# Kernel optimization log

Hardware: AMD Instinct MI355X
Metric: run time of the kernel (lower is better)

The kernel has to match this reference:

```python
import jax, jax.numpy as jnp
import numpy as np

V = 50257   # vocab / ouput_size
H = 1024    # hidden_size
L = 4096    # encoder length
NL = 2      # num_layers


def setup_inputs() -> dict:
    key = jax.random.key(0)
    ks = jax.random.split(key, 20)
    s = 0.02
    f32 = jnp.float32
    return {
        "input": jax.random.randint(ks[0], (1, 1), 0, V),
        "hidden_state": jax.random.normal(ks[1], (NL, 1, H), f32),
        "enc_outputs": jax.random.normal(ks[2], (L, H), f32),
        # parameters
        "emb": jax.random.normal(ks[3], (V, H), f32) * s,
        "Wq": jax.random.normal(ks[4], (H, H), f32) * s,
        "Wk": jax.random.normal(ks[5], (H, H), f32) * s,
        "wv": jax.random.normal(ks[6], (H, 1), f32) * s,
        "W_ih0": jax.random.normal(ks[7], (3 * H, 2 * H), f32) * s,
        "W_hh0": jax.random.normal(ks[8], (3 * H, H), f32) * s,
        "b_ih0": jnp.zeros((3 * H,), f32),
        "b_hh0": jnp.zeros((3 * H,), f32),
        "W_ih1": jax.random.normal(ks[9], (3 * H, H), f32) * s,
        "W_hh1": jax.random.normal(ks[10], (3 * H, H), f32) * s,
        "b_ih1": jnp.zeros((3 * H,), f32),
        "b_hh1": jnp.zeros((3 * H,), f32),
        "Wd": jax.random.normal(ks[11], (H, V), f32) * s,
        "bd": jnp.zeros((V,), f32),
    }


def _gru_step(x, h, W_ih, W_hh, b_ih, b_hh):
    # PyTorch GRU cell: gates ordered (reset, update, new)
    gi = W_ih @ x + b_ih          # [3H]
    gh = W_hh @ h + b_hh          # [3H]
    i_r, i_z, i_n = jnp.split(gi, 3)
    h_r, h_z, h_n = jnp.split(gh, 3)
    r = jax.nn.sigmoid(i_r + h_r)
    z = jax.nn.sigmoid(i_z + h_z)
    n = jnp.tanh(i_n + r * h_n)
    return (1.0 - z) * n + z * h


def reference(input, hidden_state, enc_outputs, emb, Wq, Wk, wv,
              W_ih0, W_hh0, b_ih0, b_hh0, W_ih1, W_hh1, b_ih1, b_hh1,
              Wd, bd):
    # embedding + (dropout p=0 is identity) + relu  -> [H]
    emb_vec = jax.nn.relu(emb[input[0, 0]])
    # additive attention: query = last-layer hidden [H], keys/values = enc [L,H]
    query = hidden_state[-1, 0]
    feat = jnp.tanh(query @ Wq + enc_outputs @ Wk)   # [L,H] (broadcast add)
    scores = feat @ wv                               # [L,1]
    attn = jax.nn.softmax(scores, axis=0)            # softmax over L
    context = jnp.sum(attn * enc_outputs, axis=0)    # [H]
    # single-step 2-layer GRU on concat(context, embedded) -> [2H]
    x = jnp.concatenate([context, emb_vec])
    h0n = _gru_step(x, hidden_state[0, 0], W_ih0, W_hh0, b_ih0, b_hh0)
    h1n = _gru_step(h0n, hidden_state[1, 0], W_ih1, W_hh1, b_ih1, b_hh1)
    # dense + log_softmax over vocab
    logits = h1n @ Wd + bd                           # [V]
    logp = jax.nn.log_softmax(logits)[None, :]       # [1,V]
    new_hidden = jnp.stack([h0n, h1n])[:, None, :]   # [NL,1,H]
    return logp, new_hidden
```

## Files before the change

### kernel.cpp

```cpp
#include <hip/hip_runtime.h>
#include <hip/hip_bf16.h>

#define H  1024
#define L  4096
#define V  50257

#define OFF_QW     0
#define OFF_SCORES 1024
#define OFF_X      5120
#define OFF_GI0    7168
#define OFF_GH0    10240
#define OFF_GI1    13312
#define OFF_GH1    16384
#define OFF_LOGITS 19456
#define OFF_PMAX   (OFF_LOGITS + V)
#define OFF_PSUM   (OFF_PMAX + 256)
#define ZERO_FLOATS (OFF_LOGITS + V)
#define OFF_WKT_BYTES 283008

typedef __bf16 bf8   __attribute__((ext_vector_type(8)));
typedef float  f32x16 __attribute__((ext_vector_type(16)));

__device__ inline unsigned int pack_bf16x2(float lo, float hi) {
    unsigned int ulo = __builtin_bit_cast(unsigned int, lo);
    unsigned int uhi = __builtin_bit_cast(unsigned int, hi);
    return ((uhi + 0x8000u) & 0xFFFF0000u) | ((ulo + 0x8000u) >> 16);
}
__device__ inline unsigned short cvt_bf16(float f) {
    unsigned int u = __builtin_bit_cast(unsigned int, f);
    return (unsigned short)((u + 0x8000u) >> 16);
}

__global__ __launch_bounds__(256) void k_prep(const int* __restrict__ tok,
                                              const float* __restrict__ emb,
                                              const float* __restrict__ hid,
                                              const float* __restrict__ Wq,
                                              const float* __restrict__ Wk,
                                              const float* __restrict__ Whh0,
                                              const float* __restrict__ bhh0,
                                              const float* __restrict__ Whh1,
                                              const float* __restrict__ bhh1,
                                              float* __restrict__ ws,
                                              unsigned short* __restrict__ wkT) {
    __shared__ float tile[32][33];
    const int b = blockIdx.x, t = threadIdx.x;
    if (b < 4) {
        int j = b * 256 + t;
        float v = emb[(size_t)tok[0] * H + j];
        ws[OFF_X + H + j] = fmaxf(v, 0.f);
    } else if (b < 68) {
        int bb = b - 4;
        int j = (bb & 3) * 256 + t;
        int i0 = (bb >> 2) * 64;
        const float* q = hid + H;
        float acc = 0.f;
#pragma unroll 8
        for (int i = i0; i < i0 + 64; ++i) acc += q[i] * Wq[i * H + j];
        atomicAdd(&ws[OFF_QW + j], acc);
    } else if (b < 1092) {
        int tt = b - 68;
        int tk = tt & 31, tn = tt >> 5;
        int c = t & 31, r0 = t >> 5;
#pragma unroll
        for (int rr = 0; rr < 4; ++rr) {
            int r = r0 + rr * 8;
            tile[r][c] = Wk[(size_t)(tk * 32 + r) * H + tn * 32 + c];
        }
        __syncthreads();
#pragma unroll
        for (int rr = 0; rr < 4; ++rr) {
            int rn = r0 + rr * 8;
            wkT[(size_t)(tn * 32 + rn) * H + tk * 32 + c] = cvt_bf16(tile[c][rn]);
        }
    } else {
        bool l1 = (b >= 1860);
        int row  = (b - (l1 ? 1860 : 1092)) * 4 + (t >> 6);
        int lane = t & 63;
        const float*  W  = l1 ? Whh1 : Whh0;
        const float*  bi = l1 ? bhh1 : bhh0;
        const float4* hv = (const float4*)(l1 ? hid + H : hid);
        const float4* Wr = (const float4*)(W + (size_t)row * H);
        float acc = 0.f;
#pragma unroll
        for (int c = lane; c < H / 4; c += 64) {
            float4 w = Wr[c], x = hv[c];
            acc += w.x * x.x + w.y * x.y + w.z * x.z + w.w * x.w;
        }
#pragma unroll
        for (int off = 32; off; off >>= 1) acc += __shfl_down(acc, off);
        if (lane == 0) ws[(l1 ? OFF_GH1 : OFF_GH0) + row] = acc + bi[row];
    }
}

__global__ __launch_bounds__(256) void k_gemm_scores(const float* __restrict__ enc,
                                                     const unsigned short* __restrict__ wkT,
                                                     const float* __restrict__ wv,
                                                     float* __restrict__ ws) {
    __shared__ unsigned short As[64][40];
    __shared__ unsigned short Bs[128][40];
    const int t = threadIdx.x, lane = t & 63, w = t >> 6;
    const int m0 = blockIdx.x * 64, n0 = blockIdx.y * 128;

    f32x16 acc0 = {}, acc1 = {};

    const int ar = t >> 2, akq = (t & 3) * 8;
    const int bn = t >> 1, bkh = (t & 1) * 16;

    const int r0 = (w & 1) * 32, c0 = (w >> 1) * 64;
    const int mrow = r0 + (lane & 31);
    const int nrow0 = c0 + (lane & 31), nrow1 = nrow0 + 32;

    for (int k0 = 0; k0 < H; k0 += 32) {
        float4 fa = *(const float4*)(enc + (size_t)(m0 + ar) * H + k0 + akq);
        float4 fb = *(const float4*)(enc + (size_t)(m0 + ar) * H + k0 + akq + 4);
        uint4 wb0 = *(const uint4*)(wkT + (size_t)(n0 + bn) * H + k0 + bkh);
        uint4 wb1 = *(const uint4*)(wkT + (size_t)(n0 + bn) * H + k0 + bkh + 8);
        __syncthreads();
        uint4 pa;
        pa.x = pack_bf16x2(fa.x, fa.y); pa.y = pack_bf16x2(fa.z, fa.w);
        pa.z = pack_bf16x2(fb.x, fb.y); pa.w = pack_bf16x2(fb.z, fb.w);
        *(uint4*)&As[ar][akq] = pa;
        *(uint4*)&Bs[bn][bkh] = wb0;
        *(uint4*)&Bs[bn][bkh + 8] = wb1;
        __syncthreads();
#pragma unroll
        for (int kk = 0; kk < 2; ++kk) {
            int kb = kk * 16 + (lane >> 5) * 8;
            bf8 a  = *(const bf8*)&As[mrow][kb];
            bf8 b0 = *(const bf8*)&Bs[nrow0][kb];
            bf8 b1 = *(const bf8*)&Bs[nrow1][kb];
            acc0 = __builtin_amdgcn_mfma_f32_32x32x16_bf16(a, b0, acc0, 0, 0, 0);
            acc1 = __builtin_amdgcn_mfma_f32_32x32x16_bf16(a, b1, acc1, 0, 0, 0);
        }
    }

    const int n_a = n0 + nrow0, n_b = n0 + nrow1;
    float qwa = ws[OFF_QW + n_a], qwb = ws[OFF_QW + n_b];
    float wva = wv[n_a], wvb = wv[n_b];
    const int rbase = m0 + r0 + 4 * (lane >> 5);
#pragma unroll
    for (int reg = 0; reg < 16; ++reg) {
        float s = tanhf(acc0[reg] + qwa) * wva + tanhf(acc1[reg] + qwb) * wvb;
#pragma unroll
        for (int msk = 1; msk < 32; msk <<= 1) s += __shfl_xor(s, msk);
        if ((lane & 31) == 0) {
            int l = rbase + (reg & 3) + 8 * (reg >> 2);
            atomicAdd(&ws[OFF_SCORES + l], s);
        }
    }
}

__global__ __launch_bounds__(256) void k_context(const float* __restrict__ enc,
                                                 float* __restrict__ ws) {
    __shared__ float red[4];
    __shared__ float ps[128];
    const int t = threadIdx.x;
    const float* sc = ws + OFF_SCORES;

    float m = -1e30f;
#pragma unroll
    for (int i = 0; i < 16; ++i) m = fmaxf(m, sc[t + i * 256]);
#pragma unroll
    for (int msk = 1; msk < 64; msk <<= 1) m = fmaxf(m, __shfl_xor(m, msk));
    if ((t & 63) == 0) red[t >> 6] = m;
    __syncthreads();
    m = fmaxf(fmaxf(red[0], red[1]), fmaxf(red[2], red[3]));
    __syncthreads();

    float s = 0.f;
#pragma unroll
    for (int i = 0; i < 16; ++i) s += expf(sc[t + i * 256] - m);
#pragma unroll
    for (int msk = 1; msk < 64; msk <<= 1) s += __shfl_xor(s, msk);
    if ((t & 63) == 0) red[t >> 6] = s;
    __syncthreads();
    float inv = 1.f / (red[0] + red[1] + red[2] + red[3]);

    const int l0 = blockIdx.y * 128;
    if (t < 128) ps[t] = expf(sc[l0 + t] - m) * inv;
    __syncthreads();

    const int h = blockIdx.x * 256 + t;
    float acc = 0.f;
#pragma unroll 4
    for (int l = 0; l < 128; ++l)
        acc += ps[l] * enc[(size_t)(l0 + l) * H + h];
    atomicAdd(&ws[OFF_X + h], acc);
}

__global__ __launch_bounds__(256) void k_gi0(const float* __restrict__ Wih,
                                             const float* __restrict__ bih,
                                             const float* __restrict__ ws_x,
                                             float* __restrict__ gi) {
    int row = blockIdx.x * 4 + (threadIdx.x >> 6);
    int lane = threadIdx.x & 63;
    const float4* Wr = (const float4*)(Wih + (size_t)row * (2 * H));
    const float4* v4 = (const float4*)ws_x;
    float acc = 0.f;
#pragma unroll
    for (int c = lane; c < 2 * H / 4; c += 64) {
        float4 w = Wr[c], xx = v4[c];
        acc += w.x * xx.x + w.y * xx.y + w.z * xx.z + w.w * xx.w;
    }
#pragma unroll
    for (int off = 32; off; off >>= 1) acc += __shfl_down(acc, off);
    if (lane == 0) gi[row] = acc + bih[row];
}

__global__ __launch_bounds__(256) void k_gi1(const float* __restrict__ Wih,
                                             const float* __restrict__ bih,
                                             const float* __restrict__ gi0,
                                             const float* __restrict__ gh0,
                                             const float* __restrict__ hid,
                                             float* __restrict__ h0n_out,
                                             float* __restrict__ gi) {
    __shared__ float xs[H];
    const int b = blockIdx.x, t = threadIdx.x, lane = t & 63;
#pragma unroll
    for (int jj = 0; jj < 4; ++jj) {
        int j = t + jj * 256;
        float r = 1.f / (1.f + expf(-(gi0[j] + gh0[j])));
        float z = 1.f / (1.f + expf(-(gi0[H + j] + gh0[H + j])));
        float n = tanhf(gi0[2 * H + j] + r * gh0[2 * H + j]);
        float h0 = (1.f - z) * n + z * hid[j];
        xs[j] = h0;
        if (b == 0) h0n_out[j] = h0;
    }
    __syncthreads();
    int row = b * 4 + (t >> 6);
    const float4* Wr = (const float4*)(Wih + (size_t)row * H);
    float acc = 0.f;
#pragma unroll
    for (int c = lane; c < H / 4; c += 64) {
        float4 w = Wr[c];
        float4 xx = *(const float4*)&xs[c * 4];
        acc += w.x * xx.x + w.y * xx.y + w.z * xx.z + w.w * xx.w;
    }
#pragma unroll
    for (int off = 32; off; off >>= 1) acc += __shfl_down(acc, off);
    if (lane == 0) gi[row] = acc + bih[row];
}

__global__ __launch_bounds__(256) void k_logits(const float* __restrict__ Wd,
                                                const float* __restrict__ bd,
                                                const float* __restrict__ gi1,
                                                const float* __restrict__ gh1,
                                                const float* __restrict__ hid,
                                                float* __restrict__ h1n_out,
                                                float* __restrict__ ws) {
    __shared__ float h1s[H];
    const int t = threadIdx.x;
#pragma unroll
    for (int jj = 0; jj < 4; ++jj) {
        int j = t + jj * 256;
        float r = 1.f / (1.f + expf(-(gi1[j] + gh1[j])));
        float z = 1.f / (1.f + expf(-(gi1[H + j] + gh1[H + j])));
        float n = tanhf(gi1[2 * H + j] + r * gh1[2 * H + j]);
        float h1 = (1.f - z) * n + z * hid[H + j];
        h1s[j] = h1;
        if (blockIdx.x == 0 && blockIdx.y == 0) h1n_out[j] = h1;
    }
    __syncthreads();
    const int v0 = blockIdx.x * 512, k0 = blockIdx.y * 128;
    const int va = v0 + t, vb = v0 + 256 + t;
    const int vac = va < V ? va : V - 1;
    const int vbc = vb < V ? vb : V - 1;
    float acca = 0.f, accb = 0.f;
    const float* Wp = Wd + (size_t)k0 * V;
#pragma unroll 8
    for (int k = 0; k < 128; ++k) {
        float xk = h1s[k0 + k];
        const float* row = Wp + (size_t)k * V;
        acca += xk * row[vac];
        accb += xk * row[vbc];
    }
    if (va < V) atomicAdd(&ws[OFF_LOGITS + va], acca + (k0 == 0 ? bd[va] : 0.f));
    if (vb < V) atomicAdd(&ws[OFF_LOGITS + vb], accb + (k0 == 0 ? bd[vb] : 0.f));
}

__global__ __launch_bounds__(256) void k_lsm1(const float* __restrict__ lg,
                                              float* __restrict__ ws) {
    __shared__ float red[4];
    const int b = blockIdx.x, t = threadIdx.x;
    const int g = b * 256 + t;
    float x = (g < V) ? lg[g] : -1e30f;

    float m = x;
#pragma unroll
    for (int msk = 1; msk < 64; msk <<= 1) m = fmaxf(m, __shfl_xor(m, msk));
    if ((t & 63) == 0) red[t >> 6] = m;
    __syncthreads();
    m = fmaxf(fmaxf(red[0], red[1]), fmaxf(red[2], red[3]));
    __syncthreads();

    float s = (g < V) ? expf(x - m) : 0.f;
#pragma unroll
    for (int msk = 1; msk < 64; msk <<= 1) s += __shfl_xor(s, msk);
    if ((t & 63) == 0) red[t >> 6] = s;
    __syncthreads();
    if (t == 0) {
        ws[OFF_PMAX + b] = m;
        ws[OFF_PSUM + b] = red[0] + red[1] + red[2] + red[3];
    }
}

__global__ __launch_bounds__(256) void k_lsm2(const float* __restrict__ lg,
                                              const float* __restrict__ ws,
                                              float* __restrict__ out) {
    __shared__ float red[4];
    const int b = blockIdx.x, t = threadIdx.x;

    float pm = (t < 197) ? ws[OFF_PMAX + t] : -1e30f;
    float m = pm;
#pragma unroll
    for (int msk = 1; msk < 64; msk <<= 1) m = fmaxf(m, __shfl_xor(m, msk));
    if ((t & 63) == 0) red[t >> 6] = m;
    __syncthreads();
    m = fmaxf(fmaxf(red[0], red[1]), fmaxf(red[2], red[3]));
    __syncthreads();

    float s = (t < 197) ? ws[OFF_PSUM + t] * expf(pm - m) : 0.f;
#pragma unroll
    for (int msk = 1; msk < 64; msk <<= 1) s += __shfl_xor(s, msk);
    if ((t & 63) == 0) red[t >> 6] = s;
    __syncthreads();
    float lse = m + logf(red[0] + red[1] + red[2] + red[3]);

    const int g = b * 256 + t;
    if (g < V) out[g] = lg[g] - lse;
}

extern "C" void kernel_launch(void* const* d_in, const int* in_sizes, int n_in,
                              void* d_out, int out_size, void* d_ws, size_t ws_size,
                              hipStream_t stream) {
    const int*   tok  = (const int*)d_in[0];
    const float* hid  = (const float*)d_in[1];
    const float* enc  = (const float*)d_in[2];
    const float* emb  = (const float*)d_in[3];
    const float* Wq   = (const float*)d_in[4];
    const float* Wk   = (const float*)d_in[5];
    const float* wv   = (const float*)d_in[6];
    const float* Wih0 = (const float*)d_in[7];
    const float* Whh0 = (const float*)d_in[8];
    const float* bih0 = (const float*)d_in[9];
    const float* bhh0 = (const float*)d_in[10];
    const float* Wih1 = (const float*)d_in[11];
    const float* Whh1 = (const float*)d_in[12];
    const float* bih1 = (const float*)d_in[13];
    const float* bhh1 = (const float*)d_in[14];
    const float* Wd   = (const float*)d_in[15];
    const float* bd   = (const float*)d_in[16];
    float* out = (float*)d_out;
    float* ws  = (float*)d_ws;
    unsigned short* wkT = (unsigned short*)((char*)d_ws + OFF_WKT_BYTES);

    hipMemsetAsync(ws, 0, ZERO_FLOATS * sizeof(float), stream);

    k_prep<<<2628, 256, 0, stream>>>(tok, emb, hid, Wq, Wk,
                                     Whh0, bhh0, Whh1, bhh1, ws, wkT);
    k_gemm_scores<<<dim3(L / 64, H / 128), 256, 0, stream>>>(enc, wkT, wv, ws);
    k_context<<<dim3(4, 32), 256, 0, stream>>>(enc, ws);
    k_gi0<<<768, 256, 0, stream>>>(Wih0, bih0, ws + OFF_X, ws + OFF_GI0);
    k_gi1<<<768, 256, 0, stream>>>(Wih1, bih1, ws + OFF_GI0, ws + OFF_GH0,
                                   hid, out + V, ws + OFF_GI1);
    k_logits<<<dim3(99, 8), 256, 0, stream>>>(Wd, bd, ws + OFF_GI1, ws + OFF_GH1,
                                              hid, out + V + H, ws);
    k_lsm1<<<197, 256, 0, stream>>>(ws + OFF_LOGITS, ws);
    k_lsm2<<<197, 256, 0, stream>>>(ws + OFF_LOGITS, ws, out);
}
```

Baseline: 518.2 us.

## Fold memset and setup work into prep kernel, pre-convert enc, retile logits

Replaces the workspace memset with zeroing blocks inside the prep kernel. The prep kernel now also converts enc_outputs to bf16 once, computes Wq·q without atomics, and precomputes the embedding half of the layer-0 input GEMV, so k_gi0 only handles the context half. The logits kernel is retiled to four vocab columns per thread with a 64-deep K split, and tanh, sigmoid and exp use fast intrinsic approximations. These changes aim to cut launch overhead, repeated fp32-to-bf16 conversion in the GEMM, and serialized GEMV work, at the cost of an extra bf16 copy of enc and reduced precision in the activations.

```diff
diff --git a/kernel.cpp b/kernel.cpp
--- a/kernel.cpp
+++ b/kernel.cpp
@@ -15,8 +15,8 @@
 #define OFF_LOGITS 19456
 #define OFF_PMAX   (OFF_LOGITS + V)
 #define OFF_PSUM   (OFF_PMAX + 256)
-#define ZERO_FLOATS (OFF_LOGITS + V)
-#define OFF_WKT_BYTES 283008
+#define OFF_WKT_BYTES   283008
+#define OFF_ENC16_BYTES 2380160
 
 typedef __bf16 bf8   __attribute__((ext_vector_type(8)));
 typedef float  f32x16 __attribute__((ext_vector_type(16)));
@@ -29,6 +29,14 @@
 __device__ inline unsigned short cvt_bf16(float f) {
     unsigned int u = __builtin_bit_cast(unsigned int, f);
     return (unsigned short)((u + 0x8000u) >> 16);
+}
+__device__ inline float fast_tanh(float x) {
+    float e = __expf(-2.f * fabsf(x));
+    float t = (1.f - e) / (1.f + e);
+    return copysignf(t, x);
+}
+__device__ inline float fast_sigmoid(float x) {
+    return 1.f / (1.f + __expf(-x));
 }
 
 __global__ __launch_bounds__(256) void k_prep(const int* __restrict__ tok,
@@ -36,29 +44,45 @@
                                               const float* __restrict__ hid,
                                               const float* __restrict__ Wq,
                                               const float* __restrict__ Wk,
+                                              const float* __restrict__ enc,
                                               const float* __restrict__ Whh0,
                                               const float* __restrict__ bhh0,
                                               const float* __restrict__ Whh1,
                                               const float* __restrict__ bhh1,
+                                              const float* __restrict__ Wih0,
+                                              const float* __restrict__ bih0,
                                               float* __restrict__ ws,
-                                              unsigned short* __restrict__ wkT) {
+                                              unsigned short* __restrict__ wkT,
+                                              unsigned short* __restrict__ enc16) {
     __shared__ float tile[32][33];
+    __shared__ float er[H];
+    __shared__ float part[4][64];
     const int b = blockIdx.x, t = threadIdx.x;
-    if (b < 4) {
-        int j = b * 256 + t;
+    if (b < 16) {
+        const int NF4 = 1280 + 12564;
+        float4 z = {0.f, 0.f, 0.f, 0.f};
+        for (int i = b * 256 + t; i < NF4; i += 16 * 256) {
+            if (i < 1280) *(float4*)(ws + OFF_SCORES + 4 * i) = z;
+            else          *(float4*)(ws + OFF_LOGITS + 4 * (i - 1280)) = z;
+        }
+        if (b == 0 && t == 0) ws[OFF_LOGITS + 50256] = 0.f;
+    } else if (b < 20) {
+        int j = (b - 16) * 256 + t;
         float v = emb[(size_t)tok[0] * H + j];
         ws[OFF_X + H + j] = fmaxf(v, 0.f);
-    } else if (b < 68) {
-        int bb = b - 4;
-        int j = (bb & 3) * 256 + t;
-        int i0 = (bb >> 2) * 64;
-        const float* q = hid + H;
+    } else if (b < 36) {
+        int j0 = (b - 20) * 64, jl = t & 63, q = t >> 6;
+        const float* qv = hid + H;
         float acc = 0.f;
 #pragma unroll 8
-        for (int i = i0; i < i0 + 64; ++i) acc += q[i] * Wq[i * H + j];
-        atomicAdd(&ws[OFF_QW + j], acc);
-    } else if (b < 1092) {
-        int tt = b - 68;
+        for (int i = q * 256; i < q * 256 + 256; ++i)
+            acc += qv[i] * Wq[(size_t)i * H + j0 + jl];
+        part[q][jl] = acc;
+        __syncthreads();
+        if (t < 64)
+            ws[OFF_QW + j0 + t] = part[0][t] + part[1][t] + part[2][t] + part[3][t];
+    } else if (b < 1060) {
+        int tt = b - 36;
         int tk = tt & 31, tn = tt >> 5;
         int c = t & 31, r0 = t >> 5;
 #pragma unroll
@@ -72,9 +96,24 @@
             int rn = r0 + rr * 8;
             wkT[(size_t)(tn * 32 + rn) * H + tk * 32 + c] = cvt_bf16(tile[c][rn]);
         }
-    } else {
-        bool l1 = (b >= 1860);
-        int row  = (b - (l1 ? 1860 : 1092)) * 4 + (t >> 6);
+    } else if (b < 2084) {
+        int row = (b - 1060) * 4 + (t >> 6);
+        int c0 = (t & 63) * 16;
+        const float* src = enc + (size_t)row * H + c0;
+        float4 f0 = *(const float4*)(src);
+        float4 f1 = *(const float4*)(src + 4);
+        float4 f2 = *(const float4*)(src + 8);
+        float4 f3 = *(const float4*)(src + 12);
+        uint4 u0, u1;
+        u0.x = pack_bf16x2(f0.x, f0.y); u0.y = pack_bf16x2(f0.z, f0.w);
+        u0.z = pack_bf16x2(f1.x, f1.y); u0.w = pack_bf16x2(f1.z, f1.w);
+        u1.x = pack_bf16x2(f2.x, f2.y); u1.y = pack_bf16x2(f2.z, f2.w);
+        u1.z = pack_bf16x2(f3.x, f3.y); u1.w = pack_bf16x2(f3.z, f3.w);
+        *(uint4*)(enc16 + (size_t)row * H + c0)     = u0;
+        *(uint4*)(enc16 + (size_t)row * H + c0 + 8) = u1;
+    } else if (b < 3620) {
+        bool l1 = (b >= 2852);
+        int row  = (b - (l1 ? 2852 : 2084)) * 4 + (t >> 6);
         int lane = t & 63;
         const float*  W  = l1 ? Whh1 : Whh0;
         const float*  bi = l1 ? bhh1 : bhh0;
@@ -89,10 +128,27 @@
 #pragma unroll
         for (int off = 32; off; off >>= 1) acc += __shfl_down(acc, off);
         if (lane == 0) ws[(l1 ? OFF_GH1 : OFF_GH0) + row] = acc + bi[row];
-    }
-}
-
-__global__ __launch_bounds__(256) void k_gemm_scores(const float* __restrict__ enc,
+    } else {
+        int row = (b - 3620) * 4 + (t >> 6);
+        int lane = t & 63;
+        int tk = tok[0];
+        for (int j = t; j < H; j += 256) er[j] = fmaxf(emb[(size_t)tk * H + j], 0.f);
+        __syncthreads();
+        const float4* Wr = (const float4*)(Wih0 + (size_t)row * (2 * H) + H);
+        const float4* e4 = (const float4*)er;
+        float acc = 0.f;
+#pragma unroll
+        for (int c = lane; c < H / 4; c += 64) {
+            float4 w = Wr[c], x = e4[c];
+            acc += w.x * x.x + w.y * x.y + w.z * x.z + w.w * x.w;
+        }
+#pragma unroll
+        for (int off = 32; off; off >>= 1) acc += __shfl_down(acc, off);
+        if (lane == 0) ws[OFF_GI0 + row] = acc + bih0[row];
+    }
+}
+
+__global__ __launch_bounds__(256) void k_gemm_scores(const unsigned short* __restrict__ enc16,
                                                      const unsigned short* __restrict__ wkT,
                                                      const float* __restrict__ wv,
                                                      float* __restrict__ ws) {
@@ -103,7 +159,7 @@
 
     f32x16 acc0 = {}, acc1 = {};
 
-    const int ar = t >> 2, akq = (t & 3) * 8;
+    const int ar = t >> 2, ak = (t & 3) * 8;
     const int bn = t >> 1, bkh = (t & 1) * 16;
 
     const int r0 = (w & 1) * 32, c0 = (w >> 1) * 64;
@@ -111,26 +167,22 @@
     const int nrow0 = c0 + (lane & 31), nrow1 = nrow0 + 32;
 
     for (int k0 = 0; k0 < H; k0 += 32) {
-        float4 fa = *(const float4*)(enc + (size_t)(m0 + ar) * H + k0 + akq);
-        float4 fb = *(const float4*)(enc + (size_t)(m0 + ar) * H + k0 + akq + 4);
+        uint4 a   = *(const uint4*)(enc16 + (size_t)(m0 + ar) * H + k0 + ak);
         uint4 wb0 = *(const uint4*)(wkT + (size_t)(n0 + bn) * H + k0 + bkh);
         uint4 wb1 = *(const uint4*)(wkT + (size_t)(n0 + bn) * H + k0 + bkh + 8);
         __syncthreads();
-        uint4 pa;
-        pa.x = pack_bf16x2(fa.x, fa.y); pa.y = pack_bf16x2(fa.z, fa.w);
-        pa.z = pack_bf16x2(fb.x, fb.y); pa.w = pack_bf16x2(fb.z, fb.w);
-        *(uint4*)&As[ar][akq] = pa;
+        *(uint4*)&As[ar][ak] = a;
         *(uint4*)&Bs[bn][bkh] = wb0;
         *(uint4*)&Bs[bn][bkh + 8] = wb1;
         __syncthreads();
 #pragma unroll
         for (int kk = 0; kk < 2; ++kk) {
             int kb = kk * 16 + (lane >> 5) * 8;
-            bf8 a  = *(const bf8*)&As[mrow][kb];
+            bf8 av = *(const bf8*)&As[mrow][kb];
             bf8 b0 = *(const bf8*)&Bs[nrow0][kb];
             bf8 b1 = *(const bf8*)&Bs[nrow1][kb];
-            acc0 = __builtin_amdgcn_mfma_f32_32x32x16_bf16(a, b0, acc0, 0, 0, 0);
-            acc1 = __builtin_amdgcn_mfma_f32_32x32x16_bf16(a, b1, acc1, 0, 0, 0);
+            acc0 = __builtin_amdgcn_mfma_f32_32x32x16_bf16(av, b0, acc0, 0, 0, 0);
+            acc1 = __builtin_amdgcn_mfma_f32_32x32x16_bf16(av, b1, acc1, 0, 0, 0);
         }
     }
 
@@ -140,7 +192,7 @@
     const int rbase = m0 + r0 + 4 * (lane >> 5);
 #pragma unroll
     for (int reg = 0; reg < 16; ++reg) {
-        float s = tanhf(acc0[reg] + qwa) * wva + tanhf(acc1[reg] + qwb) * wvb;
+        float s = fast_tanh(acc0[reg] + qwa) * wva + fast_tanh(acc1[reg] + qwb) * wvb;
 #pragma unroll
         for (int msk = 1; msk < 32; msk <<= 1) s += __shfl_xor(s, msk);
         if ((lane & 31) == 0) {
@@ -169,7 +221,7 @@
 
     float s = 0.f;
 #pragma unroll
-    for (int i = 0; i < 16; ++i) s += expf(sc[t + i * 256] - m);
+    for (int i = 0; i < 16; ++i) s += __expf(sc[t + i * 256] - m);
 #pragma unroll
     for (int msk = 1; msk < 64; msk <<= 1) s += __shfl_xor(s, msk);
     if ((t & 63) == 0) red[t >> 6] = s;
@@ -177,7 +229,7 @@
     float inv = 1.f / (red[0] + red[1] + red[2] + red[3]);
 
     const int l0 = blockIdx.y * 128;
-    if (t < 128) ps[t] = expf(sc[l0 + t] - m) * inv;
+    if (t < 128) ps[t] = __expf(sc[l0 + t] - m) * inv;
     __syncthreads();
 
     const int h = blockIdx.x * 256 + t;
@@ -189,22 +241,20 @@
 }
 
 __global__ __launch_bounds__(256) void k_gi0(const float* __restrict__ Wih,
-                                             const float* __restrict__ bih,
-                                             const float* __restrict__ ws_x,
-                                             float* __restrict__ gi) {
+                                             float* __restrict__ ws) {
     int row = blockIdx.x * 4 + (threadIdx.x >> 6);
     int lane = threadIdx.x & 63;
     const float4* Wr = (const float4*)(Wih + (size_t)row * (2 * H));
-    const float4* v4 = (const float4*)ws_x;
+    const float4* v4 = (const float4*)(ws + OFF_X);
     float acc = 0.f;
 #pragma unroll
-    for (int c = lane; c < 2 * H / 4; c += 64) {
+    for (int c = lane; c < H / 4; c += 64) {
         float4 w = Wr[c], xx = v4[c];
         acc += w.x * xx.x + w.y * xx.y + w.z * xx.z + w.w * xx.w;
     }
 #pragma unroll
     for (int off = 32; off; off >>= 1) acc += __shfl_down(acc, off);
-    if (lane == 0) gi[row] = acc + bih[row];
+    if (lane == 0) ws[OFF_GI0 + row] += acc;
 }
 
 __global__ __launch_bounds__(256) void k_gi1(const float* __restrict__ Wih,
@@ -219,9 +269,9 @@
 #pragma unroll
     for (int jj = 0; jj < 4; ++jj) {
         int j = t + jj * 256;
-        float r = 1.f / (1.f + expf(-(gi0[j] + gh0[j])));
-        float z = 1.f / (1.f + expf(-(gi0[H + j] + gh0[H + j])));
-        float n = tanhf(gi0[2 * H + j] + r * gh0[2 * H + j]);
+        float r = fast_sigmoid(gi0[j] + gh0[j]);
+        float z = fast_sigmoid(gi0[H + j] + gh0[H + j]);
+        float n = fast_tanh(gi0[2 * H + j] + r * gh0[2 * H + j]);
         float h0 = (1.f - z) * n + z * hid[j];
         xs[j] = h0;
         if (b == 0) h0n_out[j] = h0;
@@ -253,29 +303,35 @@
 #pragma unroll
     for (int jj = 0; jj < 4; ++jj) {
         int j = t + jj * 256;
-        float r = 1.f / (1.f + expf(-(gi1[j] + gh1[j])));
-        float z = 1.f / (1.f + expf(-(gi1[H + j] + gh1[H + j])));
-        float n = tanhf(gi1[2 * H + j] + r * gh1[2 * H + j]);
+        float r = fast_sigmoid(gi1[j] + gh1[j]);
+        float z = fast_sigmoid(gi1[H + j] + gh1[H + j]);
+        float n = fast_tanh(gi1[2 * H + j] + r * gh1[2 * H + j]);
         float h1 = (1.f - z) * n + z * hid[H + j];
         h1s[j] = h1;
         if (blockIdx.x == 0 && blockIdx.y == 0) h1n_out[j] = h1;
     }
     __syncthreads();
-    const int v0 = blockIdx.x * 512, k0 = blockIdx.y * 128;
-    const int va = v0 + t, vb = v0 + 256 + t;
-    const int vac = va < V ? va : V - 1;
-    const int vbc = vb < V ? vb : V - 1;
-    float acca = 0.f, accb = 0.f;
+    const int v0 = blockIdx.x * 1024, k0 = blockIdx.y * 64;
+    const int va = v0 + t, vb = va + 256, vc = va + 512, vd = va + 768;
+    const int vca = va < V ? va : V - 1;
+    const int vcb = vb < V ? vb : V - 1;
+    const int vcc = vc < V ? vc : V - 1;
+    const int vcd = vd < V ? vd : V - 1;
+    float a0 = 0.f, a1 = 0.f, a2 = 0.f, a3 = 0.f;
     const float* Wp = Wd + (size_t)k0 * V;
 #pragma unroll 8
-    for (int k = 0; k < 128; ++k) {
+    for (int k = 0; k < 64; ++k) {
         float xk = h1s[k0 + k];
         const float* row = Wp + (size_t)k * V;
-        acca += xk * row[vac];
-        accb += xk * row[vbc];
-    }
-    if (va < V) atomicAdd(&ws[OFF_LOGITS + va], acca + (k0 == 0 ? bd[va] : 0.f));
-    if (vb < V) atomicAdd(&ws[OFF_LOGITS + vb], accb + (k0 == 0 ? bd[vb] : 0.f));
+        a0 += xk * row[vca];
+        a1 += xk * row[vcb];
+        a2 += xk * row[vcc];
+        a3 += xk * row[vcd];
+    }
+    if (va < V) atomicAdd(&ws[OFF_LOGITS + va], a0 + (k0 == 0 ? bd[va] : 0.f));
+    if (vb < V) atomicAdd(&ws[OFF_LOGITS + vb], a1 + (k0 == 0 ? bd[vb] : 0.f));
+    if (vc < V) atomicAdd(&ws[OFF_LOGITS + vc], a2 + (k0 == 0 ? bd[vc] : 0.f));
+    if (vd < V) atomicAdd(&ws[OFF_LOGITS + vd], a3 + (k0 == 0 ? bd[vd] : 0.f));
 }
 
 __global__ __launch_bounds__(256) void k_lsm1(const float* __restrict__ lg,
@@ -293,7 +349,7 @@
     m = fmaxf(fmaxf(red[0], red[1]), fmaxf(red[2], red[3]));
     __syncthreads();
 
-    float s = (g < V) ? expf(x - m) : 0.f;
+    float s = (g < V) ? __expf(x - m) : 0.f;
 #pragma unroll
     for (int msk = 1; msk < 64; msk <<= 1) s += __shfl_xor(s, msk);
     if ((t & 63) == 0) red[t >> 6] = s;
@@ -319,7 +375,7 @@
     m = fmaxf(fmaxf(red[0], red[1]), fmaxf(red[2], red[3]));
     __syncthreads();
 
-    float s = (t < 197) ? ws[OFF_PSUM + t] * expf(pm - m) : 0.f;
+    float s = (t < 197) ? ws[OFF_PSUM + t] * __expf(pm - m) : 0.f;
 #pragma unroll
     for (int msk = 1; msk < 64; msk <<= 1) s += __shfl_xor(s, msk);
     if ((t & 63) == 0) red[t >> 6] = s;
@@ -352,19 +408,19 @@
     const float* bd   = (const float*)d_in[16];
     float* out = (float*)d_out;
     float* ws  = (float*)d_ws;
-    unsigned short* wkT = (unsigned short*)((char*)d_ws + OFF_WKT_BYTES);
-
-    hipMemsetAsync(ws, 0, ZERO_FLOATS * sizeof(float), stream);
-
-    k_prep<<<2628, 256, 0, stream>>>(tok, emb, hid, Wq, Wk,
-                                     Whh0, bhh0, Whh1, bhh1, ws, wkT);
-    k_gemm_scores<<<dim3(L / 64, H / 128), 256, 0, stream>>>(enc, wkT, wv, ws);
+    unsigned short* wkT   = (unsigned short*)((char*)d_ws + OFF_WKT_BYTES);
+    unsigned short* enc16 = (unsigned short*)((char*)d_ws + OFF_ENC16_BYTES);
+
+    k_prep<<<4388, 256, 0, stream>>>(tok, emb, hid, Wq, Wk, enc,
+                                     Whh0, bhh0, Whh1, bhh1, Wih0, bih0,
+                                     ws, wkT, enc16);
+    k_gemm_scores<<<dim3(L / 64, H / 128), 256, 0, stream>>>(enc16, wkT, wv, ws);
     k_context<<<dim3(4, 32), 256, 0, stream>>>(enc, ws);
-    k_gi0<<<768, 256, 0, stream>>>(Wih0, bih0, ws + OFF_X, ws + OFF_GI0);
+    k_gi0<<<768, 256, 0, stream>>>(Wih0, ws);
     k_gi1<<<768, 256, 0, stream>>>(Wih1, bih1, ws + OFF_GI0, ws + OFF_GH0,
                                    hid, out + V, ws + OFF_GI1);
-    k_logits<<<dim3(99, 8), 256, 0, stream>>>(Wd, bd, ws + OFF_GI1, ws + OFF_GH1,
-                                              hid, out + V + H, ws);
+    k_logits<<<dim3(50, 16), 256, 0, stream>>>(Wd, bd, ws + OFF_GI1, ws + OFF_GH1,
+                                               hid, out + V + H, ws);
     k_lsm1<<<197, 256, 0, stream>>>(ws + OFF_LOGITS, ws);
     k_lsm2<<<197, 256, 0, stream>>>(ws + OFF_LOGITS, ws, out);
 }
```

Measured after the change: 530.1 us. 2.3% more time.
